# Performance work log

Hardware: AMD Instinct MI355X
Metric: run time of the kernel (lower is better)

## Reference

```python
import jax, jax.numpy as jnp
import numpy as np
import math

MAX_REL_POS = 32  # max_relative_position

def _sincos_table(d_model, max_len):
    pos = np.arange(max_len)[:, None].astype(np.float32)
    div = np.exp(np.arange(0, d_model, 2).astype(np.float32) * (-math.log(10000.0) / d_model))
    pe = np.zeros((max_len, d_model), dtype=np.float32)
    pe[:, 0::2] = np.sin(pos * div)
    pe[:, 1::2] = np.cos(pos * div)
    return jnp.asarray(pe)

def setup_inputs() -> dict:
    rng = jax.random.key(0)
    k1, k2, k3 = jax.random.split(rng, 3)
    B, H, S, D = 4, 16, 1024, 64
    pe = _sincos_table(D, 2 * MAX_REL_POS + 1)  # fixed (non-trainable) buffer
    return {
        "query": jax.random.normal(k1, (B, H, S, D), jnp.float32),
        "key": jax.random.normal(k2, (B, H, S, D), jnp.float32),
        "value": jax.random.normal(k3, (B, H, S, D), jnp.float32),
        "pe_k": pe,
        "pe_v": pe,
    }

def reference(query, key, value, pe_k, pe_v):
    B, H, S, D = query.shape
    # relative distance indices: clip(k - q, -P, P) + P  -> [S, S]
    dist = jnp.clip(jnp.arange(S)[None, :] - jnp.arange(S)[:, None],
                    -MAX_REL_POS, MAX_REL_POS) + MAX_REL_POS
    R_k = pe_k[dist]  # [S, S, D]
    R_v = pe_v[dist]  # [S, S, D]
    scores = jnp.einsum('bhqd,bhkd->bhqk', query, key)
    scores = scores + jnp.einsum('bhqd,qkd->bhqk', query, R_k)
    scores = scores / math.sqrt(D)
    # one_direction=True -> causal mask
    causal = jnp.tril(jnp.ones((S, S), dtype=bool))
    scores = jnp.where(causal[None, None], scores, jnp.float32(-1e9))
    p_attn = jax.nn.softmax(scores, axis=-1)
    output = jnp.einsum('bhqk,bhkd->bhqd', p_attn, value)
    output = output + jnp.einsum('bhqv,qvd->bhqd', p_attn, R_v)
    return output, p_attn
```

## Files before the change

kernel.cpp:

```cpp
#include <hip/hip_runtime.h>

typedef __attribute__((ext_vector_type(8))) short bfrag;
typedef __attribute__((ext_vector_type(4))) float ffrag;

namespace {
constexpr int Sc = 1024, Dc = 64;
constexpr int P2 = 72;
constexpr float SCALE = 0.125f;
}

__device__ __forceinline__ unsigned short f2bf(float f) {
    unsigned u = __builtin_bit_cast(unsigned, f);
    u += 0x7fffu + ((u >> 16) & 1u);
    return (unsigned short)(u >> 16);
}
__device__ __forceinline__ bfrag pack8(float4 a, float4 b) {
    bfrag r;
    r[0] = (short)f2bf(a.x); r[1] = (short)f2bf(a.y);
    r[2] = (short)f2bf(a.z); r[3] = (short)f2bf(a.w);
    r[4] = (short)f2bf(b.x); r[5] = (short)f2bf(b.y);
    r[6] = (short)f2bf(b.z); r[7] = (short)f2bf(b.w);
    return r;
}
#define MFMA(a, b, c) __builtin_amdgcn_mfma_f32_16x16x32_bf16((a), (b), (c), 0, 0, 0)

__global__ __launch_bounds__(256, 3)
void relattn(const float* __restrict__ Qg, const float* __restrict__ Kg,
             const float* __restrict__ Vg, const float* __restrict__ pek,
             const float* __restrict__ pev, float* __restrict__ outg,
             float* __restrict__ pbuf)
{
    __shared__ __align__(16) char smem[53760];
    unsigned short* Qs = (unsigned short*)smem;
    unsigned short* Ks = (unsigned short*)(smem + 9216);
    unsigned short* Vt = (unsigned short*)(smem + 18432);
    unsigned short* Pt = (unsigned short*)(smem + 27648);
    float* Ts = (float*)(smem + 36864);
    float* Ws = (float*)(smem + 45312);
    float* W0 = (float*)(smem + 53504);
    float* Ot = (float*)(smem + 9216);

    const int tid  = threadIdx.x;
    const int bh   = blockIdx.y;
    const int wv   = tid >> 6;
    const int lane = tid & 63;
    const int n    = lane & 15;
    const int quad = lane >> 4;

    const float* Qbh = Qg + (size_t)bh * Sc * Dc;
    const float* Kbh = Kg + (size_t)bh * Sc * Dc;
    const float* Vbh = Vg + (size_t)bh * Sc * Dc;
    float* pbh = pbuf + (size_t)bh * Sc * Sc;
    float* obh = outg + (size_t)bh * Sc * Dc;

    const int sr  = tid >> 2;
    const int sc  = (tid & 3) * 16;
    const int kp  = tid & 31;
    const int vd0 = (tid >> 5) * 8;

    for (int half = 0; half < 2; ++half) {
        const int qt = half ? (15 - (int)blockIdx.x) : (int)blockIdx.x;
        const int qrow = wv * 16 + quad * 4;

        __syncthreads();

        {
            const float* src = Qbh + (size_t)(qt * 64 + sr) * Dc + sc;
            float4 a = *(const float4*)(src);
            float4 b = *(const float4*)(src + 4);
            float4 c = *(const float4*)(src + 8);
            float4 d = *(const float4*)(src + 12);
            *(bfrag*)&Qs[sr * P2 + sc]     = pack8(a, b);
            *(bfrag*)&Qs[sr * P2 + sc + 8] = pack8(c, d);
        }
        for (int idx = tid; idx < 64 * 32; idx += 256) Ws[idx] = 0.f;
        for (int i = tid; i < 135; i += 256) {
            bfrag z = {};
            *(bfrag*)&Ks[33 * P2 + i * 8] = z;
        }
        if (tid < 132) {
            int r = tid >> 2, c0 = (tid & 3) * 16;
            const float* src = pek + (size_t)r * Dc + c0;
            float4 a = *(const float4*)(src);
            float4 b = *(const float4*)(src + 4);
            float4 c = *(const float4*)(src + 8);
            float4 d = *(const float4*)(src + 12);
            *(bfrag*)&Ks[r * P2 + c0]     = pack8(a, b);
            *(bfrag*)&Ks[r * P2 + c0 + 8] = pack8(c, d);
        }
        __syncthreads();

        bfrag qa0 = *(bfrag*)&Qs[(wv * 16 + n) * P2 + quad * 8];
        bfrag qa1 = *(bfrag*)&Qs[(wv * 16 + n) * P2 + 32 + quad * 8];

        #pragma unroll
        for (int sub = 0; sub < 3; ++sub) {
            bfrag b0 = *(bfrag*)&Ks[(sub * 16 + n) * P2 + quad * 8];
            bfrag b1 = *(bfrag*)&Ks[(sub * 16 + n) * P2 + 32 + quad * 8];
            ffrag c = {};
            c = MFMA(qa0, b0, c);
            c = MFMA(qa1, b1, c);
            int j = sub * 16 + n;
            if (j <= 32) {
                #pragma unroll
                for (int reg = 0; reg < 4; ++reg)
                    Ts[(qrow + reg) * 33 + j] = c[reg];
            }
        }
        __syncthreads();

        float ts0[4];
        #pragma unroll
        for (int reg = 0; reg < 4; ++reg) ts0[reg] = Ts[(qrow + reg) * 33];

        {
            const int zb = (qt + 1) * 64;
            if (zb < Sc) {
                const int z4 = (Sc - zb) >> 2;
                const float4 z = make_float4(0.f, 0.f, 0.f, 0.f);
                for (int r = 0; r < 64; ++r) {
                    float4* rp = (float4*)(pbh + (size_t)(qt * 64 + r) * Sc + zb);
                    for (int c4 = tid; c4 < z4; c4 += 256) rp[c4] = z;
                }
            }
        }

        float lsum[4] = {0.f, 0.f, 0.f, 0.f};
        for (int kt = 0; kt <= qt; ++kt) {
            const bool bnd = (kt >= qt - 1);
            const float* ksrc = Kbh + (size_t)(kt * 64 + sr) * Dc + sc;
            float4 ka = *(const float4*)(ksrc);
            float4 kb = *(const float4*)(ksrc + 4);
            float4 kc = *(const float4*)(ksrc + 8);
            float4 kd = *(const float4*)(ksrc + 12);
            __syncthreads();
            *(bfrag*)&Ks[sr * P2 + sc]     = pack8(ka, kb);
            *(bfrag*)&Ks[sr * P2 + sc + 8] = pack8(kc, kd);
            __syncthreads();
            #pragma unroll
            for (int sub = 0; sub < 4; ++sub) {
                bfrag b0 = *(bfrag*)&Ks[(sub * 16 + n) * P2 + quad * 8];
                bfrag b1 = *(bfrag*)&Ks[(sub * 16 + n) * P2 + 32 + quad * 8];
                ffrag c = {};
                c = MFMA(qa0, b0, c);
                c = MFMA(qa1, b1, c);
                const int k = kt * 64 + sub * 16 + n;
                if (!bnd) {
                    #pragma unroll
                    for (int reg = 0; reg < 4; ++reg)
                        lsum[reg] += __expf((c[reg] + ts0[reg]) * SCALE);
                } else {
                    #pragma unroll
                    for (int reg = 0; reg < 4; ++reg) {
                        int jrel = k - (qt * 64 + qrow + reg) + 32;
                        if (jrel <= 32) {
                            int jcl = jrel < 0 ? 0 : jrel;
                            lsum[reg] += __expf((c[reg] + Ts[(qrow + reg) * 33 + jcl]) * SCALE);
                        }
                    }
                }
            }
        }
        float rinv[4];
        #pragma unroll
        for (int reg = 0; reg < 4; ++reg) {
            float l = lsum[reg];
            l += __shfl_xor(l, 1);
            l += __shfl_xor(l, 2);
            l += __shfl_xor(l, 4);
            l += __shfl_xor(l, 8);
            rinv[reg] = 1.f / l;
        }

        ffrag oacc[4];
        #pragma unroll
        for (int i = 0; i < 4; ++i) { ffrag z = {}; oacc[i] = z; }

        for (int kt = 0; kt <= qt; ++kt) {
            const bool bnd = (kt >= qt - 1);
            const float* ksrc = Kbh + (size_t)(kt * 64 + sr) * Dc + sc;
            float4 ka = *(const float4*)(ksrc);
            float4 kb = *(const float4*)(ksrc + 4);
            float4 kc = *(const float4*)(ksrc + 8);
            float4 kd = *(const float4*)(ksrc + 12);
            const float* vsrc = Vbh + (size_t)(kt * 64 + 2 * kp) * Dc + vd0;
            float4 v0a = *(const float4*)(vsrc);
            float4 v0b = *(const float4*)(vsrc + 4);
            float4 v1a = *(const float4*)(vsrc + Dc);
            float4 v1b = *(const float4*)(vsrc + Dc + 4);
            __syncthreads();
            *(bfrag*)&Ks[sr * P2 + sc]     = pack8(ka, kb);
            *(bfrag*)&Ks[sr * P2 + sc + 8] = pack8(kc, kd);
            {
                float r0[8] = {v0a.x, v0a.y, v0a.z, v0a.w, v0b.x, v0b.y, v0b.z, v0b.w};
                float r1[8] = {v1a.x, v1a.y, v1a.z, v1a.w, v1b.x, v1b.y, v1b.z, v1b.w};
                #pragma unroll
                for (int i = 0; i < 8; ++i) {
                    unsigned pk = (unsigned)f2bf(r0[i]) | ((unsigned)f2bf(r1[i]) << 16);
                    *(unsigned*)&Vt[(vd0 + i) * P2 + 2 * kp] = pk;
                }
            }
            __syncthreads();
            #pragma unroll
            for (int sub = 0; sub < 4; ++sub) {
                bfrag b0 = *(bfrag*)&Ks[(sub * 16 + n) * P2 + quad * 8];
                bfrag b1 = *(bfrag*)&Ks[(sub * 16 + n) * P2 + 32 + quad * 8];
                ffrag c = {};
                c = MFMA(qa0, b0, c);
                c = MFMA(qa1, b1, c);
                const int k = kt * 64 + sub * 16 + n;
                float* prow = pbh + (size_t)(qt * 64 + qrow) * Sc + k;
                if (!bnd) {
                    #pragma unroll
                    for (int reg = 0; reg < 4; ++reg) {
                        float p = __expf((c[reg] + ts0[reg]) * SCALE) * rinv[reg];
                        prow[(size_t)reg * Sc] = p;
                        Pt[(qrow + reg) * P2 + sub * 16 + n] = (unsigned short)f2bf(p);
                    }
                } else {
                    #pragma unroll
                    for (int reg = 0; reg < 4; ++reg) {
                        int jrel = k - (qt * 64 + qrow + reg) + 32;
                        float p = 0.f;
                        if (jrel <= 32) {
                            int jcl = jrel < 0 ? 0 : jrel;
                            p = __expf((c[reg] + Ts[(qrow + reg) * 33 + jcl]) * SCALE) * rinv[reg];
                        }
                        prow[(size_t)reg * Sc] = p;
                        Pt[(qrow + reg) * P2 + sub * 16 + n] = (unsigned short)f2bf(p);
                        if ((unsigned)(jrel - 1) < 32u) Ws[(qrow + reg) * 32 + jrel - 1] = p;
                    }
                }
            }
            __syncthreads();
            bfrag pb0 = *(bfrag*)&Pt[(wv * 16 + n) * P2 + quad * 8];
            bfrag pb1 = *(bfrag*)&Pt[(wv * 16 + n) * P2 + 32 + quad * 8];
            #pragma unroll
            for (int ds = 0; ds < 4; ++ds) {
                bfrag va0 = *(bfrag*)&Vt[(ds * 16 + n) * P2 + quad * 8];
                bfrag va1 = *(bfrag*)&Vt[(ds * 16 + n) * P2 + 32 + quad * 8];
                oacc[ds] = MFMA(va0, pb0, oacc[ds]);
                oacc[ds] = MFMA(va1, pb1, oacc[ds]);
            }
        }

        __syncthreads();
        if (tid < 64) {
            float s = 0.f;
            #pragma unroll
            for (int j = 0; j < 32; ++j) s += Ws[tid * 32 + j];
            W0[tid] = 1.f - s;
        }
        {
            int q = tid >> 2, j0 = (tid & 3) * 8;
            #pragma unroll
            for (int i = 0; i < 8; i += 2) {
                unsigned pk = (unsigned)f2bf(Ws[q * 32 + j0 + i]) |
                              ((unsigned)f2bf(Ws[q * 32 + j0 + i + 1]) << 16);
                *(unsigned*)&Pt[q * P2 + j0 + i] = pk;
            }
        }
        {
            int jj = tid >> 3, d0 = (tid & 7) * 8;
            const float* src = pev + (size_t)(jj + 1) * Dc + d0;
            float4 a = *(const float4*)(src);
            float4 b = *(const float4*)(src + 4);
            float vr[8] = {a.x, a.y, a.z, a.w, b.x, b.y, b.z, b.w};
            #pragma unroll
            for (int i = 0; i < 8; ++i)
                Vt[(d0 + i) * P2 + jj] = (unsigned short)f2bf(vr[i]);
        }
        __syncthreads();
        {
            bfrag pb = *(bfrag*)&Pt[(wv * 16 + n) * P2 + quad * 8];
            #pragma unroll
            for (int ds = 0; ds < 4; ++ds) {
                bfrag va = *(bfrag*)&Vt[(ds * 16 + n) * P2 + quad * 8];
                oacc[ds] = MFMA(va, pb, oacc[ds]);
            }
        }
        float w0q = W0[wv * 16 + n];
        __syncthreads();
        #pragma unroll
        for (int ds = 0; ds < 4; ++ds) {
            float4 ov;
            ov.x = oacc[ds][0] + w0q * pev[ds * 16 + quad * 4 + 0];
            ov.y = oacc[ds][1] + w0q * pev[ds * 16 + quad * 4 + 1];
            ov.z = oacc[ds][2] + w0q * pev[ds * 16 + quad * 4 + 2];
            ov.w = oacc[ds][3] + w0q * pev[ds * 16 + quad * 4 + 3];
            *(float4*)&Ot[(wv * 16 + n) * 68 + ds * 16 + quad * 4] = ov;
        }
        __syncthreads();
        {
            int r = tid >> 2, c0 = (tid & 3) * 16;
            float* dst = obh + (size_t)(qt * 64 + r) * Dc + c0;
            *(float4*)(dst)      = *(float4*)&Ot[r * 68 + c0];
            *(float4*)(dst + 4)  = *(float4*)&Ot[r * 68 + c0 + 4];
            *(float4*)(dst + 8)  = *(float4*)&Ot[r * 68 + c0 + 8];
            *(float4*)(dst + 12) = *(float4*)&Ot[r * 68 + c0 + 12];
        }
    }
}

extern "C" void kernel_launch(void* const* d_in, const int* in_sizes, int n_in,
                              void* d_out, int out_size, void* d_ws, size_t ws_size,
                              hipStream_t stream)
{
    const float* Q   = (const float*)d_in[0];
    const float* K   = (const float*)d_in[1];
    const float* V   = (const float*)d_in[2];
    const float* pek = (const float*)d_in[3];
    const float* pev = (const float*)d_in[4];
    float* out  = (float*)d_out;
    float* pbuf = out + (size_t)64 * Sc * Dc;

    dim3 grid(8, 64);
    relattn<<<grid, 256, 0, stream>>>(Q, K, V, pek, pev, out, pbuf);
}
```

Before: 391.5 us.

## Load Q/K fragments directly from global and double-buffer P/V tiles

Q, K and the positional-key table are now loaded straight from global memory into MFMA register fragments instead of being staged through shared memory. This removes two barriers per key tile in both passes. The P and V staging buffers in the second pass are double-buffered so only one barrier per tile remains. Occupancy hint drops from 3 to 2 blocks per CU to allow more registers. The trade-off is redundant, less coalesced global reads of K rows per wave, with reuse now depending on cache.

```diff
diff --git a/kernel.cpp b/kernel.cpp
--- a/kernel.cpp
+++ b/kernel.cpp
@@ -22,23 +22,26 @@
     r[6] = (short)f2bf(b.z); r[7] = (short)f2bf(b.w);
     return r;
 }
+__device__ __forceinline__ bfrag load_row8(const float* p) {
+    float4 a = *(const float4*)(p);
+    float4 b = *(const float4*)(p + 4);
+    return pack8(a, b);
+}
 #define MFMA(a, b, c) __builtin_amdgcn_mfma_f32_16x16x32_bf16((a), (b), (c), 0, 0, 0)
 
-__global__ __launch_bounds__(256, 3)
+__global__ __launch_bounds__(256, 2)
 void relattn(const float* __restrict__ Qg, const float* __restrict__ Kg,
              const float* __restrict__ Vg, const float* __restrict__ pek,
              const float* __restrict__ pev, float* __restrict__ outg,
              float* __restrict__ pbuf)
 {
     __shared__ __align__(16) char smem[53760];
-    unsigned short* Qs = (unsigned short*)smem;
-    unsigned short* Ks = (unsigned short*)(smem + 9216);
-    unsigned short* Vt = (unsigned short*)(smem + 18432);
-    unsigned short* Pt = (unsigned short*)(smem + 27648);
+    unsigned short* PtA = (unsigned short*)smem;
+    unsigned short* VtA = (unsigned short*)(smem + 18432);
     float* Ts = (float*)(smem + 36864);
     float* Ws = (float*)(smem + 45312);
     float* W0 = (float*)(smem + 53504);
-    float* Ot = (float*)(smem + 9216);
+    float* Ot = (float*)smem;
 
     const int tid  = threadIdx.x;
     const int bh   = blockIdx.y;
@@ -53,8 +56,6 @@
     float* pbh = pbuf + (size_t)bh * Sc * Sc;
     float* obh = outg + (size_t)bh * Sc * Dc;
 
-    const int sr  = tid >> 2;
-    const int sc  = (tid & 3) * 16;
     const int kp  = tid & 31;
     const int vd0 = (tid >> 5) * 8;
 
@@ -64,43 +65,21 @@
 
         __syncthreads();
 
-        {
-            const float* src = Qbh + (size_t)(qt * 64 + sr) * Dc + sc;
-            float4 a = *(const float4*)(src);
-            float4 b = *(const float4*)(src + 4);
-            float4 c = *(const float4*)(src + 8);
-            float4 d = *(const float4*)(src + 12);
-            *(bfrag*)&Qs[sr * P2 + sc]     = pack8(a, b);
-            *(bfrag*)&Qs[sr * P2 + sc + 8] = pack8(c, d);
-        }
+        const float* qsrc = Qbh + (size_t)(qt * 64 + wv * 16 + n) * Dc;
+        bfrag qa0 = load_row8(qsrc + quad * 8);
+        bfrag qa1 = load_row8(qsrc + 32 + quad * 8);
+
         for (int idx = tid; idx < 64 * 32; idx += 256) Ws[idx] = 0.f;
-        for (int i = tid; i < 135; i += 256) {
-            bfrag z = {};
-            *(bfrag*)&Ks[33 * P2 + i * 8] = z;
-        }
-        if (tid < 132) {
-            int r = tid >> 2, c0 = (tid & 3) * 16;
-            const float* src = pek + (size_t)r * Dc + c0;
-            float4 a = *(const float4*)(src);
-            float4 b = *(const float4*)(src + 4);
-            float4 c = *(const float4*)(src + 8);
-            float4 d = *(const float4*)(src + 12);
-            *(bfrag*)&Ks[r * P2 + c0]     = pack8(a, b);
-            *(bfrag*)&Ks[r * P2 + c0 + 8] = pack8(c, d);
-        }
-        __syncthreads();
-
-        bfrag qa0 = *(bfrag*)&Qs[(wv * 16 + n) * P2 + quad * 8];
-        bfrag qa1 = *(bfrag*)&Qs[(wv * 16 + n) * P2 + 32 + quad * 8];
 
         #pragma unroll
         for (int sub = 0; sub < 3; ++sub) {
-            bfrag b0 = *(bfrag*)&Ks[(sub * 16 + n) * P2 + quad * 8];
-            bfrag b1 = *(bfrag*)&Ks[(sub * 16 + n) * P2 + 32 + quad * 8];
+            int j = sub * 16 + n;
+            const float* psrc = pek + (size_t)j * Dc;
+            bfrag b0 = load_row8(psrc + quad * 8);
+            bfrag b1 = load_row8(psrc + 32 + quad * 8);
             ffrag c = {};
             c = MFMA(qa0, b0, c);
             c = MFMA(qa1, b1, c);
-            int j = sub * 16 + n;
             if (j <= 32) {
                 #pragma unroll
                 for (int reg = 0; reg < 4; ++reg)
@@ -128,23 +107,15 @@
         float lsum[4] = {0.f, 0.f, 0.f, 0.f};
         for (int kt = 0; kt <= qt; ++kt) {
             const bool bnd = (kt >= qt - 1);
-            const float* ksrc = Kbh + (size_t)(kt * 64 + sr) * Dc + sc;
-            float4 ka = *(const float4*)(ksrc);
-            float4 kb = *(const float4*)(ksrc + 4);
-            float4 kc = *(const float4*)(ksrc + 8);
-            float4 kd = *(const float4*)(ksrc + 12);
-            __syncthreads();
-            *(bfrag*)&Ks[sr * P2 + sc]     = pack8(ka, kb);
-            *(bfrag*)&Ks[sr * P2 + sc + 8] = pack8(kc, kd);
-            __syncthreads();
             #pragma unroll
             for (int sub = 0; sub < 4; ++sub) {
-                bfrag b0 = *(bfrag*)&Ks[(sub * 16 + n) * P2 + quad * 8];
-                bfrag b1 = *(bfrag*)&Ks[(sub * 16 + n) * P2 + 32 + quad * 8];
+                const int k = kt * 64 + sub * 16 + n;
+                const float* krow = Kbh + (size_t)k * Dc;
+                bfrag b0 = load_row8(krow + quad * 8);
+                bfrag b1 = load_row8(krow + 32 + quad * 8);
                 ffrag c = {};
                 c = MFMA(qa0, b0, c);
                 c = MFMA(qa1, b1, c);
-                const int k = kt * 64 + sub * 16 + n;
                 if (!bnd) {
                     #pragma unroll
                     for (int reg = 0; reg < 4; ++reg)
@@ -176,46 +147,34 @@
         #pragma unroll
         for (int i = 0; i < 4; ++i) { ffrag z = {}; oacc[i] = z; }
 
+        int bsel = 0;
         for (int kt = 0; kt <= qt; ++kt) {
             const bool bnd = (kt >= qt - 1);
-            const float* ksrc = Kbh + (size_t)(kt * 64 + sr) * Dc + sc;
-            float4 ka = *(const float4*)(ksrc);
-            float4 kb = *(const float4*)(ksrc + 4);
-            float4 kc = *(const float4*)(ksrc + 8);
-            float4 kd = *(const float4*)(ksrc + 12);
+            unsigned short* Ptb = PtA + bsel * 4608;
+            unsigned short* Vtb = VtA + bsel * 4608;
+
             const float* vsrc = Vbh + (size_t)(kt * 64 + 2 * kp) * Dc + vd0;
             float4 v0a = *(const float4*)(vsrc);
             float4 v0b = *(const float4*)(vsrc + 4);
             float4 v1a = *(const float4*)(vsrc + Dc);
             float4 v1b = *(const float4*)(vsrc + Dc + 4);
-            __syncthreads();
-            *(bfrag*)&Ks[sr * P2 + sc]     = pack8(ka, kb);
-            *(bfrag*)&Ks[sr * P2 + sc + 8] = pack8(kc, kd);
-            {
-                float r0[8] = {v0a.x, v0a.y, v0a.z, v0a.w, v0b.x, v0b.y, v0b.z, v0b.w};
-                float r1[8] = {v1a.x, v1a.y, v1a.z, v1a.w, v1b.x, v1b.y, v1b.z, v1b.w};
-                #pragma unroll
-                for (int i = 0; i < 8; ++i) {
-                    unsigned pk = (unsigned)f2bf(r0[i]) | ((unsigned)f2bf(r1[i]) << 16);
-                    *(unsigned*)&Vt[(vd0 + i) * P2 + 2 * kp] = pk;
-                }
-            }
-            __syncthreads();
+
             #pragma unroll
             for (int sub = 0; sub < 4; ++sub) {
-                bfrag b0 = *(bfrag*)&Ks[(sub * 16 + n) * P2 + quad * 8];
-                bfrag b1 = *(bfrag*)&Ks[(sub * 16 + n) * P2 + 32 + quad * 8];
+                const int k = kt * 64 + sub * 16 + n;
+                const float* krow = Kbh + (size_t)k * Dc;
+                bfrag b0 = load_row8(krow + quad * 8);
+                bfrag b1 = load_row8(krow + 32 + quad * 8);
                 ffrag c = {};
                 c = MFMA(qa0, b0, c);
                 c = MFMA(qa1, b1, c);
-                const int k = kt * 64 + sub * 16 + n;
                 float* prow = pbh + (size_t)(qt * 64 + qrow) * Sc + k;
                 if (!bnd) {
                     #pragma unroll
                     for (int reg = 0; reg < 4; ++reg) {
                         float p = __expf((c[reg] + ts0[reg]) * SCALE) * rinv[reg];
                         prow[(size_t)reg * Sc] = p;
-                        Pt[(qrow + reg) * P2 + sub * 16 + n] = (unsigned short)f2bf(p);
+                        Ptb[(qrow + reg) * P2 + sub * 16 + n] = (unsigned short)f2bf(p);
                     }
                 } else {
                     #pragma unroll
@@ -227,21 +186,32 @@
                             p = __expf((c[reg] + Ts[(qrow + reg) * 33 + jcl]) * SCALE) * rinv[reg];
                         }
                         prow[(size_t)reg * Sc] = p;
-                        Pt[(qrow + reg) * P2 + sub * 16 + n] = (unsigned short)f2bf(p);
+                        Ptb[(qrow + reg) * P2 + sub * 16 + n] = (unsigned short)f2bf(p);
                         if ((unsigned)(jrel - 1) < 32u) Ws[(qrow + reg) * 32 + jrel - 1] = p;
                     }
                 }
             }
+            {
+                float r0[8] = {v0a.x, v0a.y, v0a.z, v0a.w, v0b.x, v0b.y, v0b.z, v0b.w};
+                float r1[8] = {v1a.x, v1a.y, v1a.z, v1a.w, v1b.x, v1b.y, v1b.z, v1b.w};
+                #pragma unroll
+                for (int i = 0; i < 8; ++i) {
+                    unsigned pk = (unsigned)f2bf(r0[i]) | ((unsigned)f2bf(r1[i]) << 16);
+                    *(unsigned*)&Vtb[(vd0 + i) * P2 + 2 * kp] = pk;
+                }
+            }
             __syncthreads();
-            bfrag pb0 = *(bfrag*)&Pt[(wv * 16 + n) * P2 + quad * 8];
-            bfrag pb1 = *(bfrag*)&Pt[(wv * 16 + n) * P2 + 32 + quad * 8];
+
+            bfrag pb0 = *(bfrag*)&Ptb[(wv * 16 + n) * P2 + quad * 8];
+            bfrag pb1 = *(bfrag*)&Ptb[(wv * 16 + n) * P2 + 32 + quad * 8];
             #pragma unroll
             for (int ds = 0; ds < 4; ++ds) {
-                bfrag va0 = *(bfrag*)&Vt[(ds * 16 + n) * P2 + quad * 8];
-                bfrag va1 = *(bfrag*)&Vt[(ds * 16 + n) * P2 + 32 + quad * 8];
+                bfrag va0 = *(bfrag*)&Vtb[(ds * 16 + n) * P2 + quad * 8];
+                bfrag va1 = *(bfrag*)&Vtb[(ds * 16 + n) * P2 + 32 + quad * 8];
                 oacc[ds] = MFMA(va0, pb0, oacc[ds]);
                 oacc[ds] = MFMA(va1, pb1, oacc[ds]);
             }
+            bsel ^= 1;
         }
 
         __syncthreads();
@@ -257,7 +227,7 @@
             for (int i = 0; i < 8; i += 2) {
                 unsigned pk = (unsigned)f2bf(Ws[q * 32 + j0 + i]) |
                               ((unsigned)f2bf(Ws[q * 32 + j0 + i + 1]) << 16);
-                *(unsigned*)&Pt[q * P2 + j0 + i] = pk;
+                *(unsigned*)&PtA[q * P2 + j0 + i] = pk;
             }
         }
         {
@@ -268,14 +238,14 @@
             float vr[8] = {a.x, a.y, a.z, a.w, b.x, b.y, b.z, b.w};
             #pragma unroll
             for (int i = 0; i < 8; ++i)
-                Vt[(d0 + i) * P2 + jj] = (unsigned short)f2bf(vr[i]);
-        }
-        __syncthreads();
-        {
-            bfrag pb = *(bfrag*)&Pt[(wv * 16 + n) * P2 + quad * 8];
+                VtA[(d0 + i) * P2 + jj] = (unsigned short)f2bf(vr[i]);
+        }
+        __syncthreads();
+        {
+            bfrag pb = *(bfrag*)&PtA[(wv * 16 + n) * P2 + quad * 8];
             #pragma unroll
             for (int ds = 0; ds < 4; ++ds) {
-                bfrag va = *(bfrag*)&Vt[(ds * 16 + n) * P2 + quad * 8];
+                bfrag va = *(bfrag*)&VtA[(ds * 16 + n) * P2 + quad * 8];
                 oacc[ds] = MFMA(va, pb, oacc[ds]);
             }
         }
```

Result: slower. 460.4 us (+17.6%).
